# Kernel tuning notes

Hardware: AMD Instinct MI355X
Metric: run time of the kernel (lower is better)

## Reference

```python
import jax, jax.numpy as jnp
import numpy as np

HEADS = 48
HEAD_DIM = 64
DIM = 3072
RANK = 128
TEXT_LEN = 226
VID_LEN = 1822
B = 1
LORA_W = 1.0
EPS = 1e-5


def setup_inputs() -> dict:
    key = jax.random.key(0)
    ks = jax.random.split(key, 24)
    s = 0.02  # weight init scale
    inp = {
        "hidden_states": jax.random.normal(ks[0], (B, VID_LEN, DIM), jnp.float32),
        "encoder_hidden_states": jax.random.normal(ks[1], (B, TEXT_LEN, DIM), jnp.float32),
        "rope_cos": jax.random.uniform(ks[2], (VID_LEN, HEAD_DIM), jnp.float32),
        "rope_sin": jax.random.uniform(ks[3], (VID_LEN, HEAD_DIM), jnp.float32),
        "Wq": jax.random.normal(ks[4], (DIM, DIM), jnp.float32) * s,
        "bq": jax.random.normal(ks[5], (DIM,), jnp.float32) * s,
        "Wk": jax.random.normal(ks[6], (DIM, DIM), jnp.float32) * s,
        "bk": jax.random.normal(ks[7], (DIM,), jnp.float32) * s,
        "Wv": jax.random.normal(ks[8], (DIM, DIM), jnp.float32) * s,
        "bv": jax.random.normal(ks[9], (DIM,), jnp.float32) * s,
        "Wo": jax.random.normal(ks[10], (DIM, DIM), jnp.float32) * s,
        "bo": jax.random.normal(ks[11], (DIM,), jnp.float32) * s,
        "lq_down": jax.random.normal(ks[12], (RANK, DIM), jnp.float32) / RANK,
        "lq_up": jax.random.normal(ks[13], (DIM, RANK), jnp.float32) * s,
        "lk_down": jax.random.normal(ks[14], (RANK, DIM), jnp.float32) / RANK,
        "lk_up": jax.random.normal(ks[15], (DIM, RANK), jnp.float32) * s,
        "lv_down": jax.random.normal(ks[16], (RANK, DIM), jnp.float32) / RANK,
        "lv_up": jax.random.normal(ks[17], (DIM, RANK), jnp.float32) * s,
        "lp_down": jax.random.normal(ks[18], (RANK, DIM), jnp.float32) / RANK,
        "lp_up": jax.random.normal(ks[19], (DIM, RANK), jnp.float32) * s,
        "gamma_q": jnp.ones((HEAD_DIM,), jnp.float32),
        "beta_q": jnp.zeros((HEAD_DIM,), jnp.float32),
        "gamma_k": jnp.ones((HEAD_DIM,), jnp.float32),
        "beta_k": jnp.zeros((HEAD_DIM,), jnp.float32),
    }
    return inp


def _lora(x, down, up):
    # x: [B,S,DIM]; down: [RANK,DIM]; up: [DIM,RANK]
    return (x @ down.T) @ up.T


def _layernorm(x, gamma, beta):
    mu = jnp.mean(x, axis=-1, keepdims=True)
    var = jnp.mean(jnp.square(x - mu), axis=-1, keepdims=True)
    return (x - mu) * jax.lax.rsqrt(var + EPS) * gamma + beta


def _apply_rope(x, cos, sin):
    # diffusers apply_rotary_emb, use_real=True, unbind_dim=-1
    # x: [B,H,S,D]; cos/sin: [S,D]
    xr = x.reshape(*x.shape[:-1], HEAD_DIM // 2, 2)
    x1, x2 = xr[..., 0], xr[..., 1]
    x_rot = jnp.stack([-x2, x1], axis=-1).reshape(x.shape)
    return x * cos + x_rot * sin


def reference(hidden_states, encoder_hidden_states, rope_cos, rope_sin,
              Wq, bq, Wk, bk, Wv, bv, Wo, bo,
              lq_down, lq_up, lk_down, lk_up, lv_down, lv_up, lp_down, lp_up,
              gamma_q, beta_q, gamma_k, beta_k):
    h = jnp.concatenate([encoder_hidden_states, hidden_states], axis=1)  # [B,S,DIM]
    S = h.shape[1]

    q = h @ Wq.T + bq + _lora(h, lq_down, lq_up) * LORA_W
    k = h @ Wk.T + bk + _lora(h, lk_down, lk_up) * LORA_W
    v = h @ Wv.T + bv + _lora(h, lv_down, lv_up) * LORA_W

    def split_heads(x):  # [B,S,DIM] -> [B,H,S,D]
        return x.reshape(B, S, HEADS, HEAD_DIM).transpose(0, 2, 1, 3)

    q, k, v = split_heads(q), split_heads(k), split_heads(v)
    q = _layernorm(q, gamma_q, beta_q)
    k = _layernorm(k, gamma_k, beta_k)

    # RoPE on video tokens only
    q = q.at[:, :, TEXT_LEN:].set(_apply_rope(q[:, :, TEXT_LEN:], rope_cos, rope_sin))
    k = k.at[:, :, TEXT_LEN:].set(_apply_rope(k[:, :, TEXT_LEN:], rope_cos, rope_sin))

    # scaled dot-product attention (no mask, no dropout)
    scale = 1.0 / np.sqrt(HEAD_DIM).astype(np.float32)
    scores = jnp.einsum("bhqd,bhkd->bhqk", q, k) * scale
    probs = jax.nn.softmax(scores, axis=-1)
    attn_out = jnp.einsum("bhqk,bhkd->bhqd", probs, v)

    out = attn_out.transpose(0, 2, 1, 3).reshape(B, S, DIM)
    out = out @ Wo.T + bo + _lora(out, lp_down, lp_up) * LORA_W

    enc_out = out[:, :TEXT_LEN, :]
    hid_out = out[:, TEXT_LEN:, :]
    return (hid_out, enc_out)
```

## Files before the change

### kernel.cpp

```cpp
#include <hip/hip_runtime.h>
#include <hip/hip_bf16.h>
#include <stdint.h>

#define S_TOT 2048
#define TEXT 226
#define VID 1822
#define DIM 3072
#define NH 48
#define HD 64

typedef __bf16 bf16x8 __attribute__((ext_vector_type(8)));
typedef __bf16 bf16x4 __attribute__((ext_vector_type(4)));
typedef float f32x4 __attribute__((ext_vector_type(4)));

#define AS1 __attribute__((address_space(1)))
#define AS3 __attribute__((address_space(3)))

__device__ __forceinline__ void g2l16(const void* g, void* l) {
    __builtin_amdgcn_global_load_lds((const AS1 uint32_t*)(uintptr_t)g,
                                     (AS3 uint32_t*)(uintptr_t)l, 16, 0, 0);
}

__device__ __forceinline__ f32x4 mfma16(bf16x4 a, bf16x4 b, f32x4 c) {
#if __has_builtin(__builtin_amdgcn_mfma_f32_16x16x16bf16_1k)
    typedef short s4 __attribute__((ext_vector_type(4)));
    union U { bf16x4 b; s4 s; };
    U ua, ub; ua.b = a; ub.b = b;
    return __builtin_amdgcn_mfma_f32_16x16x16bf16_1k(ua.s, ub.s, c, 0, 0, 0);
#else
    f32x4 d = c;
    asm volatile("v_mfma_f32_16x16x16_bf16 %0, %1, %2, %0"
                 : "+v"(d) : "v"(a), "v"(b));
    return d;
#endif
}

#define ARENA_N 47431680ull

struct NormArgs { const void* p[24]; };

__global__ __launch_bounds__(256)
void normalize_inputs(NormArgs a, __bf16* __restrict__ arena)
{
    static constexpr unsigned long long segStart[25] = {
        0ull, 694272ull, 6291456ull, 15728640ull, 25165824ull, 34603008ull,
        44040192ull, 44433408ull, 44826624ull, 45219840ull, 45613056ull,
        46006272ull, 46399488ull, 46792704ull, 47185920ull, 47302528ull,
        47419136ull, 47422208ull, 47425280ull, 47428352ull, 47431424ull,
        47431488ull, 47431552ull, 47431616ull, 47431680ull };
    static constexpr int segIn[24] = {
        1, 0, 4, 6, 8, 10, 12, 13, 14, 15, 16, 17, 18, 19, 2, 3,
        5, 7, 9, 11, 20, 21, 22, 23 };

    const uint32_t w0 = *(const uint32_t*)a.p[20];
    const bool f32in = (w0 == 0x3F800000u);

    const size_t i0 = ((size_t)blockIdx.x * 256 + threadIdx.x) * 8;
    if (i0 >= ARENA_N) return;
    int s = 0;
    while (i0 >= segStart[s + 1]) s++;
    const size_t off = i0 - segStart[s];

    if (f32in) {
        const float* src = (const float*)a.p[segIn[s]] + off;
        const float4 v0 = ((const float4*)src)[0];
        const float4 v1 = ((const float4*)src)[1];
        bf16x8 o;
        o[0] = (__bf16)v0.x; o[1] = (__bf16)v0.y; o[2] = (__bf16)v0.z; o[3] = (__bf16)v0.w;
        o[4] = (__bf16)v1.x; o[5] = (__bf16)v1.y; o[6] = (__bf16)v1.z; o[7] = (__bf16)v1.w;
        *(bf16x8*)(arena + i0) = o;
    } else {
        const __bf16* src = (const __bf16*)a.p[segIn[s]] + off;
        *(uint4*)(arena + i0) = *(const uint4*)src;
    }
}

__device__ __forceinline__ void mm_chunks(
    const __bf16* __restrict__ Ag, int lda, const __bf16* __restrict__ Bg, int ldb,
    int kbeg, int kend, f32x4 (&acc)[4][4], __bf16* As, __bf16* Bs,
    int wave, int srow, int schk, int rdoff, int l15, int wm, int wn)
{
    for (int k0 = kbeg; k0 < kend; k0 += 32) {
        __syncthreads();
#pragma unroll
        for (int i = 0; i < 2; i++) {
            const int blk = i * 4 + wave;
            const int r = blk * 16 + srow;
            g2l16(Ag + (size_t)r * lda + k0 + schk, &As[blk * 512]);
            g2l16(Bg + (size_t)r * ldb + k0 + schk, &Bs[blk * 512]);
        }
        __syncthreads();
        bf16x8 af[4], bfr[4];
#pragma unroll
        for (int i = 0; i < 4; i++)
            af[i] = *(const bf16x8*)&As[(wm + i * 16 + l15) * 32 + rdoff];
#pragma unroll
        for (int j = 0; j < 4; j++)
            bfr[j] = *(const bf16x8*)&Bs[(wn + j * 16 + l15) * 32 + rdoff];
#pragma unroll
        for (int i = 0; i < 4; i++)
#pragma unroll
            for (int j = 0; j < 4; j++)
                acc[i][j] = __builtin_amdgcn_mfma_f32_16x16x32_bf16(af[i], bfr[j], acc[i][j], 0, 0, 0);
    }
}

template<int MODE>
__global__ __launch_bounds__(256)
void gemm_bt(const __bf16* __restrict__ A, int lda,
             const __bf16* __restrict__ B0, const __bf16* __restrict__ B1,
             const __bf16* __restrict__ B2, int ldb,
             const __bf16* __restrict__ bias0, const __bf16* __restrict__ bias1,
             const __bf16* __restrict__ bias2,
             __bf16* __restrict__ Cb, int ldc, int K, int tilesPerGroup,
             void* __restrict__ dout, const void* __restrict__ probe)
{
    __shared__ __bf16 As[128 * 32];
    __shared__ __bf16 Bs[128 * 32];
    const int tid  = threadIdx.x;
    const int wave = tid >> 6;
    const int lane = tid & 63;
    const int l15  = lane & 15, quad = lane >> 4;
    const int bm = blockIdx.x, bn = blockIdx.y;
    const int group = bn / tilesPerGroup;
    const int nt    = bn - group * tilesPerGroup;
    const __bf16* B    = (group == 0) ? B0 : ((group == 1) ? B1 : B2);
    const __bf16* bias = (group == 0) ? bias0 : ((group == 1) ? bias1 : bias2);

    const int srow  = lane >> 2;
    const int schk  = ((((lane & 3) - (lane >> 3)) & 3)) * 8;
    const int rdoff = ((quad + (l15 >> 1)) & 3) * 8;
    const __bf16* Ag = A + (size_t)(bm * 128) * lda;
    const __bf16* Bg = B + (size_t)(nt * 128) * ldb;

    f32x4 acc[4][4] = {};
    const int wm = (wave & 1) * 64;
    const int wn = (wave >> 1) * 64;

    mm_chunks(Ag, lda, Bg, ldb, 0, K, acc, As, Bs, wave, srow, schk, rdoff, l15, wm, wn);

    bool f32out = false;
    if (MODE == 1) f32out = (*(const uint32_t*)probe == 0x3F800000u);

#pragma unroll
    for (int i = 0; i < 4; i++) {
#pragma unroll
        for (int j = 0; j < 4; j++) {
            const int coll = wn + j * 16 + l15;
            const int col  = bn * 128 + coll;
            float bv = 0.f;
            if (bias) bv = (float)bias[nt * 128 + coll];
#pragma unroll
            for (int r = 0; r < 4; r++) {
                const int row = bm * 128 + wm + i * 16 + quad * 4 + r;
                float v = acc[i][j][r] + bv;
                if (MODE == 1) {
                    const size_t mrow = (row < TEXT) ? (size_t)(row + VID) : (size_t)(row - TEXT);
                    if (f32out) ((float*)dout)[mrow * DIM + col] = v;
                    else        ((__bf16*)dout)[mrow * DIM + col] = (__bf16)v;
                } else {
                    Cb[(size_t)row * ldc + col] = (__bf16)v;
                }
            }
        }
    }
}

#define QKV_NT 48
#define QKV_NI 24

__device__ __forceinline__ void barx() {
    asm volatile("" ::: "memory");
    __builtin_amdgcn_s_barrier();
    asm volatile("" ::: "memory");
}
__device__ __forceinline__ void vmw6() { asm volatile("s_waitcnt vmcnt(6)" ::: "memory"); }
__device__ __forceinline__ void vmw0() { asm volatile("s_waitcnt vmcnt(0)" ::: "memory"); }

__device__ __forceinline__ void stage2(const __bf16* gsrc, __bf16* lds, size_t koff) {
    g2l16(gsrc + koff,      lds);
    g2l16(gsrc + koff + 32, lds + 8192);
}

__global__ __launch_bounds__(512)
void gemm256_qkv(const __bf16* __restrict__ A,
                 const __bf16* __restrict__ B0, const __bf16* __restrict__ B1,
                 const __bf16* __restrict__ B2,
                 const __bf16* __restrict__ bias0, const __bf16* __restrict__ bias1,
                 const __bf16* __restrict__ bias2,
                 __bf16* __restrict__ C)
{
    __shared__ __bf16 L[65536];

    const int bid = blockIdx.x;
    const int swz = (bid & 7) * 32 + (bid >> 3);
    const int bm = swz & 7;
    const int bn = swz >> 3;
    const int group = bn / 12;
    const int nt    = bn - group * 12;
    const __bf16* Bm   = (group == 0) ? B0 : ((group == 1) ? B1 : B2);
    const __bf16* bias = (group == 0) ? bias0 : ((group == 1) ? bias1 : bias2);

    const int tid = threadIdx.x, wave = tid >> 6, lane = tid & 63;
    const int wr = wave >> 2, wc = wave & 3;
    const int l15 = lane & 15, quad = lane >> 4;
    const int srow  = lane >> 2;
    const int schk  = ((((lane & 3) - (lane >> 3)) & 3)) * 8;
    const int rdoff = ((quad + (l15 >> 1)) & 3) * 8;
    const int rdbase = l15 * 32 + rdoff;

    static constexpr int AL0[8] = {0,1,2,3, 8,9,10,11};
    static constexpr int AL1[8] = {4,5,6,7, 12,13,14,15};
    static constexpr int BL0[8] = {0,1,4,5, 8,9,12,13};
    static constexpr int BL1[8] = {2,3,6,7, 10,11,14,15};
    const int a0 = AL0[wave], a1 = AL1[wave], b0 = BL0[wave], b1 = BL1[wave];

    const __bf16* Ag = A  + (size_t)(bm * 256) * DIM;
    const __bf16* Bg = Bm + (size_t)(nt * 256) * DIM;
    const __bf16* gA0 = Ag + (size_t)(a0 * 16 + srow) * DIM + schk;
    const __bf16* gA1 = Ag + (size_t)(a1 * 16 + srow) * DIM + schk;
    const __bf16* gB0 = Bg + (size_t)(b0 * 16 + srow) * DIM + schk;
    const __bf16* gB1 = Bg + (size_t)(b1 * 16 + srow) * DIM + schk;

#define STG_A0(BUF, T) stage2(gA0, &L[(BUF)*32768 +         a0*512], (size_t)(T)*64)
#define STG_A1(BUF, T) stage2(gA1, &L[(BUF)*32768 +         a1*512], (size_t)(T)*64)
#define STG_B0(BUF, T) stage2(gB0, &L[(BUF)*32768 + 16384 + b0*512], (size_t)(T)*64)
#define STG_B1(BUF, T) stage2(gB1, &L[(BUF)*32768 + 16384 + b1*512], (size_t)(T)*64)

    f32x4 acc[8][4] = {};

    STG_A0(0, 0); STG_B0(0, 0); STG_A1(0, 0); STG_B1(0, 0);
    STG_A0(1, 1); STG_B0(1, 1); STG_A1(1, 1);
    vmw6();
    barx();

#define PH(BUF, MH, NH, STAGE, WAIT) do {                                        \
    bf16x8 af[4][2], bfr[2][2];                                                  \
    _Pragma("unroll")                                                            \
    for (int mm = 0; mm < 4; mm++) {                                             \
        af[mm][0] = *(const bf16x8*)&L[(BUF)*32768 +        (wr*8 + (MH)*4 + mm)*512 + rdbase]; \
        af[mm][1] = *(const bf16x8*)&L[(BUF)*32768 + 8192 + (wr*8 + (MH)*4 + mm)*512 + rdbase]; \
    }                                                                            \
    _Pragma("unroll")                                                            \
    for (int nn = 0; nn < 2; nn++) {                                             \
        bfr[nn][0] = *(const bf16x8*)&L[(BUF)*32768 + 16384 +        (wc*4 + (NH)*2 + nn)*512 + rdbase]; \
        bfr[nn][1] = *(const bf16x8*)&L[(BUF)*32768 + 16384 + 8192 + (wc*4 + (NH)*2 + nn)*512 + rdbase]; \
    }                                                                            \
    barx();                                                                      \
    STAGE;                                                                       \
    __builtin_amdgcn_s_setprio(1);                                               \
    _Pragma("unroll")                                                            \
    for (int mm = 0; mm < 4; mm++)                                               \
        _Pragma("unroll")                                                        \
        for (int nn = 0; nn < 2; nn++) {                                         \
            acc[(MH)*4+mm][(NH)*2+nn] = __builtin_amdgcn_mfma_f32_16x16x32_bf16( \
                af[mm][0], bfr[nn][0], acc[(MH)*4+mm][(NH)*2+nn], 0, 0, 0);      \
            acc[(MH)*4+mm][(NH)*2+nn] = __builtin_amdgcn_mfma_f32_16x16x32_bf16( \
                af[mm][1], bfr[nn][1], acc[(MH)*4+mm][(NH)*2+nn], 0, 0, 0);      \
        }                                                                        \
    __builtin_amdgcn_s_setprio(0);                                               \
    WAIT;                                                                        \
    barx();                                                                      \
} while (0)

#pragma unroll 1
    for (int i = 0; i < QKV_NI; i++) {
        const int t1 = 2 * i + 1, t2 = 2 * i + 2, t3 = 2 * i + 3;
        const bool more = (i < QKV_NI - 1);
        PH(0, 0, 0, { STG_B1(1, t1); },              { });
        PH(0, 0, 1, { if (more) STG_A0(0, t2); },    { });
        PH(0, 1, 0, { if (more) STG_B0(0, t2); },    { });
        PH(0, 1, 1, { if (more) STG_A1(0, t2); },    { if (more) vmw6(); else vmw0(); });
        PH(1, 0, 0, { if (more) STG_B1(0, t2); },    { });
        PH(1, 0, 1, { if (more) STG_A0(1, t3); },    { });
        PH(1, 1, 0, { if (more) STG_B0(1, t3); },    { });
        PH(1, 1, 1, { if (more) STG_A1(1, t3); },    { if (more) vmw6(); else vmw0(); });
    }
#undef PH
#undef STG_A0
#undef STG_A1
#undef STG_B0
#undef STG_B1

#pragma unroll
    for (int mh = 0; mh < 2; mh++)
#pragma unroll
    for (int nh = 0; nh < 2; nh++)
#pragma unroll
    for (int nn = 0; nn < 2; nn++) {
        const int coll = wc * 64 + nh * 32 + nn * 16 + l15;
        const float bv = (float)bias[nt * 256 + coll];
        const int col = bn * 256 + coll;
#pragma unroll
        for (int mm = 0; mm < 4; mm++) {
            const int rowb = bm * 256 + wr * 128 + mh * 64 + mm * 16 + quad * 4;
#pragma unroll
            for (int r = 0; r < 4; r++)
                C[(size_t)(rowb + r) * 9216 + col] = (__bf16)(acc[mh*4+mm][nh*2+nn][r] + bv);
        }
    }
}

struct TpArgs { const __bf16* S[4]; __bf16* D[4]; };

__global__ __launch_bounds__(256)
void transp_ld(TpArgs a)
{
    __shared__ float tile[64][65];
    const __bf16* src = a.S[blockIdx.z];
    __bf16* dst = a.D[blockIdx.z];
    const int j0 = blockIdx.x * 64;
    const int r0 = blockIdx.y * 64;
    const int tid = threadIdx.x;
    const int rr = tid >> 4;
    const int cc = (tid & 15) * 4;
#pragma unroll
    for (int p = 0; p < 4; p++) {
        const int r = p * 16 + rr;
        const uint2 raw = *(const uint2*)&src[(size_t)(r0 + r) * DIM + j0 + cc];
        const __bf16* b = (const __bf16*)&raw;
#pragma unroll
        for (int e = 0; e < 4; e++) tile[r][cc + e] = (float)b[e];
    }
    __syncthreads();
#pragma unroll
    for (int p = 0; p < 4; p++) {
        const int j = p * 16 + rr;
        __bf16 o[4];
#pragma unroll
        for (int e = 0; e < 4; e++) o[e] = (__bf16)tile[cc + e][j];
        *(uint2*)&dst[(size_t)(j0 + j) * 128 + r0 + cc] = *(const uint2*)o;
    }
}

struct FoldArgs { const __bf16* A[4]; const __bf16* B[4]; const __bf16* W[4]; __bf16* D[4]; };

__global__ __launch_bounds__(256)
void fold_w(FoldArgs a)
{
    __shared__ __bf16 As[128 * 32];
    __shared__ __bf16 Bs[128 * 32];
    const int z = blockIdx.z;
    const int tid  = threadIdx.x;
    const int wave = tid >> 6;
    const int lane = tid & 63;
    const int l15  = lane & 15, quad = lane >> 4;
    const int bm = blockIdx.x, bn = blockIdx.y;

    const int srow  = lane >> 2;
    const int schk  = ((((lane & 3) - (lane >> 3)) & 3)) * 8;
    const int rdoff = ((quad + (l15 >> 1)) & 3) * 8;
    const __bf16* Ag = a.A[z] + (size_t)(bm * 128) * 128;
    const __bf16* Bg = a.B[z] + (size_t)(bn * 128) * 128;
    const __bf16* W  = a.W[z];
    __bf16* D = a.D[z];

    f32x4 acc[4][4] = {};
    const int wm = (wave & 1) * 64;
    const int wn = (wave >> 1) * 64;

    mm_chunks(Ag, 128, Bg, 128, 0, 128, acc, As, Bs, wave, srow, schk, rdoff, l15, wm, wn);

#pragma unroll
    for (int i = 0; i < 4; i++) {
#pragma unroll
        for (int j = 0; j < 4; j++) {
            const int col = bn * 128 + wn + j * 16 + l15;
#pragma unroll
            for (int r = 0; r < 4; r++) {
                const int row = bm * 128 + wm + i * 16 + quad * 4 + r;
                const size_t idx = (size_t)row * DIM + col;
                D[idx] = (__bf16)(acc[i][j][r] + (float)W[idx]);
            }
        }
    }
}

__global__ __launch_bounds__(256)
void ln_vt(const __bf16* __restrict__ qkv,
           const __bf16* __restrict__ gq, const __bf16* __restrict__ bq,
           const __bf16* __restrict__ gk, const __bf16* __restrict__ bk,
           const __bf16* __restrict__ cosb, const __bf16* __restrict__ sinb,
           __bf16* __restrict__ qh, __bf16* __restrict__ kh,
           __bf16* __restrict__ vt)
{
    __shared__ float tile[64][65];
    if (blockIdx.x < 2048) {
        const int s = blockIdx.x;
        const int wave = threadIdx.x >> 6, lane = threadIdx.x & 63;
        for (int idx = wave; idx < 2 * NH; idx += 4) {
            const int mat  = idx / NH;
            const int head = idx - mat * NH;
            float x = (float)qkv[(size_t)s * 9216 + mat * DIM + head * HD + lane];
            float mu = x;
            mu += __shfl_xor(mu, 1, 64);  mu += __shfl_xor(mu, 2, 64);
            mu += __shfl_xor(mu, 4, 64);  mu += __shfl_xor(mu, 8, 64);
            mu += __shfl_xor(mu, 16, 64); mu += __shfl_xor(mu, 32, 64);
            mu *= 0.015625f;
            float d = x - mu;
            float vv = d * d;
            vv += __shfl_xor(vv, 1, 64);  vv += __shfl_xor(vv, 2, 64);
            vv += __shfl_xor(vv, 4, 64);  vv += __shfl_xor(vv, 8, 64);
            vv += __shfl_xor(vv, 16, 64); vv += __shfl_xor(vv, 32, 64);
            vv *= 0.015625f;
            const float g = (float)(mat ? gk[lane] : gq[lane]);
            const float b = (float)(mat ? bk[lane] : bq[lane]);
            float y = d * rsqrtf(vv + 1e-5f) * g + b;
            if (s >= TEXT) {
                const int pos = s - TEXT;
                const float c  = (float)cosb[pos * HD + lane];
                const float sn = (float)sinb[pos * HD + lane];
                const float oth = __shfl_xor(y, 1, 64);
                const float rot = (lane & 1) ? oth : -oth;
                y = y * c + rot * sn;
            }
            if (mat == 0) y *= 0.125f;
            __bf16* dst = mat ? kh : qh;
            dst[((size_t)head * S_TOT + s) * HD + lane] = (__bf16)y;
        }
    } else {
        const int vb = blockIdx.x - 2048;
        const int h = vb >> 5, sb = vb & 31;
        const int tid = threadIdx.x;
        const int r0 = tid >> 4;
        const int c0 = (tid & 15) * 4;
#pragma unroll
        for (int p = 0; p < 4; p++) {
            const int r = p * 16 + r0;
            const uint2 raw = *(const uint2*)&qkv[((size_t)(sb * 64 + r)) * 9216 + 2 * DIM + h * HD + c0];
            const __bf16* b = (const __bf16*)&raw;
#pragma unroll
            for (int e = 0; e < 4; e++) tile[r][c0 + e] = (float)b[e];
        }
        __syncthreads();
#pragma unroll
        for (int p = 0; p < 4; p++) {
            const int d = p * 16 + r0;
            __bf16 o[4];
#pragma unroll
            for (int e = 0; e < 4; e++) o[e] = (__bf16)tile[c0 + e][d];
            *(uint2*)&vt[((size_t)(h * HD + d)) * S_TOT + sb * 64 + c0] = *(const uint2*)o;
        }
    }
}

#define KS_LD 72
#define VS_LD 136
#define NKB (S_TOT / 128)

__device__ __forceinline__ void fa_load(const __bf16* __restrict__ kh,
                                        const __bf16* __restrict__ vt,
                                        int h, int kb, int tid,
                                        bf16x8 (&kr)[4], bf16x8 (&vr)[4])
{
#pragma unroll
    for (int p = 0; p < 4; p++) {
        const int id = p * 256 + tid;
        const int krow = id >> 3, kc = (id & 7) * 8;
        kr[p] = *(const bf16x8*)(kh + ((size_t)(h * S_TOT + kb * 128 + krow)) * HD + kc);
        const int vrow = id >> 4, vc = (id & 15) * 8;
        vr[p] = *(const bf16x8*)(vt + ((size_t)(h * HD + vrow)) * S_TOT + kb * 128 + vc);
    }
}

__global__ __launch_bounds__(256)
void flash_attn(const __bf16* __restrict__ qh, const __bf16* __restrict__ kh,
                const __bf16* __restrict__ vt, __bf16* __restrict__ outp)
{
    __shared__ __bf16 Ks[128 * KS_LD];
    __shared__ __bf16 Vs[64 * VS_LD];
    const int qb = blockIdx.x, h = blockIdx.y;
    const int tid = threadIdx.x, wave = tid >> 6, lane = tid & 63;
    const int l15 = lane & 15, quad = lane >> 4;

    const __bf16* qp = qh + ((size_t)(h * S_TOT + qb * 64 + wave * 16 + l15)) * HD + quad * 8;
    const bf16x8 qf0 = *(const bf16x8*)qp;
    const bf16x8 qf1 = *(const bf16x8*)(qp + 32);

    f32x4 of[4] = {};
    float m_i = -1e30f, l_i = 0.f;
    const float L2E = 1.44269504f;

    bf16x8 kr[4], vr[4];
    fa_load(kh, vt, h, 0, tid, kr, vr);

    for (int kb = 0; kb < NKB; kb++) {
        __syncthreads();
#pragma unroll
        for (int p = 0; p < 4; p++) {
            const int id = p * 256 + tid;
            const int krow = id >> 3, kc = (id & 7) * 8;
            *(bf16x8*)&Ks[krow * KS_LD + kc] = kr[p];
            const int vrow = id >> 4, vc = (id & 15) * 8;
            *(bf16x8*)&Vs[vrow * VS_LD + vc] = vr[p];
        }
        __syncthreads();
        if (kb + 1 < NKB) fa_load(kh, vt, h, kb + 1, tid, kr, vr);

        f32x4 sf[8];
#pragma unroll
        for (int n = 0; n < 8; n++) {
            const bf16x8 k0 = *(const bf16x8*)&Ks[(n * 16 + l15) * KS_LD + quad * 8];
            const bf16x8 k1 = *(const bf16x8*)&Ks[(n * 16 + l15) * KS_LD + 32 + quad * 8];
            f32x4 z = {0.f, 0.f, 0.f, 0.f};
            z = __builtin_amdgcn_mfma_f32_16x16x32_bf16(k0, qf0, z, 0, 0, 0);
            sf[n] = __builtin_amdgcn_mfma_f32_16x16x32_bf16(k1, qf1, z, 0, 0, 0);
        }

        float mx = sf[0][0];
#pragma unroll
        for (int n = 0; n < 8; n++)
#pragma unroll
            for (int r = 0; r < 4; r++) mx = fmaxf(mx, sf[n][r]);
        mx = fmaxf(mx, __shfl_xor(mx, 16, 64));
        mx = fmaxf(mx, __shfl_xor(mx, 32, 64));
        const float mnew = fmaxf(m_i, mx);
        const float alpha = __builtin_amdgcn_exp2f((m_i - mnew) * L2E);
        m_i = mnew;
        float rs = 0.f;
#pragma unroll
        for (int n = 0; n < 8; n++)
#pragma unroll
            for (int r = 0; r < 4; r++) {
                const float pv = __builtin_amdgcn_exp2f((sf[n][r] - mnew) * L2E);
                sf[n][r] = pv;
                rs += pv;
            }
        rs += __shfl_xor(rs, 16, 64);
        rs += __shfl_xor(rs, 32, 64);
        l_i = l_i * alpha + rs;

        bf16x4 pf[8];
#pragma unroll
        for (int kk = 0; kk < 8; kk++) {
            bf16x4 o;
            o[0] = (__bf16)sf[kk][0]; o[1] = (__bf16)sf[kk][1];
            o[2] = (__bf16)sf[kk][2]; o[3] = (__bf16)sf[kk][3];
            pf[kk] = o;
        }

#pragma unroll
        for (int r = 0; r < 4; r++) {
            const float a_r = __shfl(alpha, quad * 4 + r, 16);
#pragma unroll
            for (int j = 0; j < 4; j++) of[j][r] *= a_r;
        }

#pragma unroll
        for (int kk = 0; kk < 8; kk++) {
#pragma unroll
            for (int j = 0; j < 4; j++) {
                const bf16x4 vf = *(const bf16x4*)&Vs[(j * 16 + l15) * VS_LD + kk * 16 + quad * 4];
                of[j] = mfma16(pf[kk], vf, of[j]);
            }
        }
    }

#pragma unroll
    for (int r = 0; r < 4; r++) {
        const float lr = __shfl(l_i, quad * 4 + r, 16);
        const float inv = 1.f / lr;
        const int row = qb * 64 + wave * 16 + quad * 4 + r;
#pragma unroll
        for (int j = 0; j < 4; j++)
            outp[(size_t)row * DIM + h * HD + j * 16 + l15] = (__bf16)(of[j][r] * inv);
    }
}

extern "C" void kernel_launch(void* const* d_in, const int* in_sizes, int n_in,
                              void* d_out, int out_size, void* d_ws, size_t ws_size,
                              hipStream_t stream)
{
    char* ws = (char*)d_ws;
    __bf16* arena = (__bf16*)ws;

    const __bf16* h     = arena + 0;
    const __bf16* Wq    = arena + 6291456;
    const __bf16* Wk    = arena + 15728640;
    const __bf16* Wv    = arena + 25165824;
    const __bf16* Wo    = arena + 34603008;
    const __bf16* lqd   = arena + 44040192;
    const __bf16* lqu   = arena + 44433408;
    const __bf16* lkd   = arena + 44826624;
    const __bf16* lku   = arena + 45219840;
    const __bf16* lvd   = arena + 45613056;
    const __bf16* lvu   = arena + 46006272;
    const __bf16* lpd   = arena + 46399488;
    const __bf16* lpu   = arena + 46792704;
    const __bf16* ropec = arena + 47185920;
    const __bf16* ropes = arena + 47302528;
    const __bf16* bq    = arena + 47419136;
    const __bf16* bk    = arena + 47422208;
    const __bf16* bv    = arena + 47425280;
    const __bf16* bo    = arena + 47428352;
    const __bf16* gq    = arena + 47431424;
    const __bf16* btq   = arena + 47431488;
    const __bf16* gk    = arena + 47431552;
    const __bf16* btk   = arena + 47431616;

    __bf16* ldT  = (__bf16*)(ws + 94863360);
    __bf16* qkvb = (__bf16*)(ws + 98009088);
    __bf16* Wpo  = (__bf16*)(ws + 135757824);
    __bf16* Wpq  = (__bf16*)(ws + 154632192);
    __bf16* Wpk  = (__bf16*)(ws + 173506560);
    __bf16* Wpv  = (__bf16*)(ws + 192380928);
    __bf16* qh   = (__bf16*)(ws + 154632192);
    __bf16* kh   = (__bf16*)(ws + 179798016);
    __bf16* vt   = (__bf16*)(ws + 12582912);
    __bf16* attn = (__bf16*)(ws + 0);

    NormArgs na;
    for (int i = 0; i < 24; i++) na.p[i] = d_in[i];
    normalize_inputs<<<(unsigned)((ARENA_N / 8 + 255) / 256), 256, 0, stream>>>(na, arena);

    TpArgs tp;
    tp.S[0] = lqd; tp.S[1] = lkd; tp.S[2] = lvd; tp.S[3] = lpd;
    tp.D[0] = ldT; tp.D[1] = ldT + 393216; tp.D[2] = ldT + 786432; tp.D[3] = ldT + 1179648;
    transp_ld<<<dim3(48, 2, 4), 256, 0, stream>>>(tp);

    FoldArgs fa;
    fa.A[0] = lqu; fa.A[1] = lku; fa.A[2] = lvu; fa.A[3] = lpu;
    fa.B[0] = tp.D[0]; fa.B[1] = tp.D[1]; fa.B[2] = tp.D[2]; fa.B[3] = tp.D[3];
    fa.W[0] = Wq; fa.W[1] = Wk; fa.W[2] = Wv; fa.W[3] = Wo;
    fa.D[0] = Wpq; fa.D[1] = Wpk; fa.D[2] = Wpv; fa.D[3] = Wpo;
    fold_w<<<dim3(24, 24, 4), 256, 0, stream>>>(fa);

    gemm256_qkv<<<256, 512, 0, stream>>>(h, Wpq, Wpk, Wpv, bq, bk, bv, qkvb);
    gemm_bt<3><<<dim3(16, 8), 256, 0, stream>>>(
        h, DIM, Wpv + (size_t)2048 * DIM, Wpv + (size_t)2048 * DIM, Wpv + (size_t)2048 * DIM,
        DIM, bv + 2048, bv + 2048, bv + 2048,
        qkvb + 8192, 9216, DIM, 8, nullptr, nullptr);

    ln_vt<<<2048 + 1536, 256, 0, stream>>>(qkvb, gq, btq, gk, btk, ropec, ropes, qh, kh, vt);

    flash_attn<<<dim3(32, 48), 256, 0, stream>>>(qh, kh, vt, attn);

    gemm_bt<1><<<dim3(16, 24), 256, 0, stream>>>(
        attn, DIM, Wpo, Wpo, Wpo, DIM, bo, bo, bo,
        nullptr, DIM, DIM, 24, d_out, d_in[20]);
}
```

Before: 712.7 us.

## Process two query tiles per flash-attention block and fold log2e into Q scale

Each flash-attention block now handles 128 query rows as two 64-row passes that share each staged K/V tile, halving the grid and the K/V global-to-LDS traffic per query. The softmax scale now includes log2(e) in the Q prescale, which removes the per-element multiply before exp2. Launch bounds request 3 blocks per CU. The cost is more registers for two sets of accumulators and fewer blocks (768) to spread across CUs.

```diff
diff --git a/kernel.cpp b/kernel.cpp
--- a/kernel.cpp
+++ b/kernel.cpp
@@ -414,7 +414,7 @@
                 const float rot = (lane & 1) ? oth : -oth;
                 y = y * c + rot * sn;
             }
-            if (mat == 0) y *= 0.125f;
+            if (mat == 0) y *= 0.1803368801111137f;
             __bf16* dst = mat ? kh : qh;
             dst[((size_t)head * S_TOT + s) * HD + lane] = (__bf16)y;
         }
@@ -463,23 +463,89 @@
     }
 }
 
-__global__ __launch_bounds__(256)
+__device__ __forceinline__ void fa_pass(const __bf16* __restrict__ Ks,
+                                        const __bf16* __restrict__ Vs,
+                                        bf16x8 qf0, bf16x8 qf1,
+                                        f32x4 (&of)[4], float& m_i, float& l_i,
+                                        int l15, int quad)
+{
+    f32x4 sf[8];
+#pragma unroll
+    for (int n = 0; n < 8; n++) {
+        const bf16x8 k0 = *(const bf16x8*)&Ks[(n * 16 + l15) * KS_LD + quad * 8];
+        const bf16x8 k1 = *(const bf16x8*)&Ks[(n * 16 + l15) * KS_LD + 32 + quad * 8];
+        f32x4 z = {0.f, 0.f, 0.f, 0.f};
+        z = __builtin_amdgcn_mfma_f32_16x16x32_bf16(k0, qf0, z, 0, 0, 0);
+        sf[n] = __builtin_amdgcn_mfma_f32_16x16x32_bf16(k1, qf1, z, 0, 0, 0);
+    }
+
+    float mx = fmaxf(fmaxf(sf[0][0], sf[0][1]), fmaxf(sf[0][2], sf[0][3]));
+#pragma unroll
+    for (int n = 1; n < 8; n++)
+        mx = fmaxf(mx, fmaxf(fmaxf(sf[n][0], sf[n][1]), fmaxf(sf[n][2], sf[n][3])));
+    mx = fmaxf(mx, __shfl_xor(mx, 16, 64));
+    mx = fmaxf(mx, __shfl_xor(mx, 32, 64));
+    const float mnew = fmaxf(m_i, mx);
+    const float alpha = __builtin_amdgcn_exp2f(m_i - mnew);
+    m_i = mnew;
+    float rs = 0.f;
+#pragma unroll
+    for (int n = 0; n < 8; n++)
+#pragma unroll
+        for (int r = 0; r < 4; r++) {
+            const float pv = __builtin_amdgcn_exp2f(sf[n][r] - mnew);
+            sf[n][r] = pv;
+            rs += pv;
+        }
+    rs += __shfl_xor(rs, 16, 64);
+    rs += __shfl_xor(rs, 32, 64);
+    l_i = l_i * alpha + rs;
+
+    bf16x4 pf[8];
+#pragma unroll
+    for (int kk = 0; kk < 8; kk++) {
+        bf16x4 o;
+        o[0] = (__bf16)sf[kk][0]; o[1] = (__bf16)sf[kk][1];
+        o[2] = (__bf16)sf[kk][2]; o[3] = (__bf16)sf[kk][3];
+        pf[kk] = o;
+    }
+
+#pragma unroll
+    for (int r = 0; r < 4; r++) {
+        const float a_r = __shfl(alpha, quad * 4 + r, 16);
+#pragma unroll
+        for (int j = 0; j < 4; j++) of[j][r] *= a_r;
+    }
+
+#pragma unroll
+    for (int kk = 0; kk < 8; kk++) {
+#pragma unroll
+        for (int j = 0; j < 4; j++) {
+            const bf16x4 vf = *(const bf16x4*)&Vs[(j * 16 + l15) * VS_LD + kk * 16 + quad * 4];
+            of[j] = mfma16(pf[kk], vf, of[j]);
+        }
+    }
+}
+
+__global__ __launch_bounds__(256, 3)
 void flash_attn(const __bf16* __restrict__ qh, const __bf16* __restrict__ kh,
                 const __bf16* __restrict__ vt, __bf16* __restrict__ outp)
 {
     __shared__ __bf16 Ks[128 * KS_LD];
     __shared__ __bf16 Vs[64 * VS_LD];
-    const int qb = blockIdx.x, h = blockIdx.y;
+    const int qb2 = blockIdx.x, h = blockIdx.y;
     const int tid = threadIdx.x, wave = tid >> 6, lane = tid & 63;
     const int l15 = lane & 15, quad = lane >> 4;
 
-    const __bf16* qp = qh + ((size_t)(h * S_TOT + qb * 64 + wave * 16 + l15)) * HD + quad * 8;
-    const bf16x8 qf0 = *(const bf16x8*)qp;
-    const bf16x8 qf1 = *(const bf16x8*)(qp + 32);
-
-    f32x4 of[4] = {};
-    float m_i = -1e30f, l_i = 0.f;
-    const float L2E = 1.44269504f;
+    const __bf16* qp = qh + ((size_t)(h * S_TOT + qb2 * 128 + wave * 16 + l15)) * HD + quad * 8;
+    const bf16x8 qf0a = *(const bf16x8*)qp;
+    const bf16x8 qf1a = *(const bf16x8*)(qp + 32);
+    const bf16x8 qf0b = *(const bf16x8*)(qp + 64 * HD);
+    const bf16x8 qf1b = *(const bf16x8*)(qp + 64 * HD + 32);
+
+    f32x4 ofa[4] = {}, ofb[4] = {};
+    float m_a = -1e30f, l_a = 0.f;
+    float m_b = -1e30f, l_b = 0.f;
 
     bf16x8 kr[4], vr[4];
     fa_load(kh, vt, h, 0, tid, kr, vr);
@@ -495,75 +561,26 @@
             *(bf16x8*)&Vs[vrow * VS_LD + vc] = vr[p];
         }
         __syncthreads();
+
+        fa_pass(Ks, Vs, qf0a, qf1a, ofa, m_a, l_a, l15, quad);
         if (kb + 1 < NKB) fa_load(kh, vt, h, kb + 1, tid, kr, vr);
-
-        f32x4 sf[8];
-#pragma unroll
-        for (int n = 0; n < 8; n++) {
-            const bf16x8 k0 = *(const bf16x8*)&Ks[(n * 16 + l15) * KS_LD + quad * 8];
-            const bf16x8 k1 = *(const bf16x8*)&Ks[(n * 16 + l15) * KS_LD + 32 + quad * 8];
-            f32x4 z = {0.f, 0.f, 0.f, 0.f};
-            z = __builtin_amdgcn_mfma_f32_16x16x32_bf16(k0, qf0, z, 0, 0, 0);
-            sf[n] = __builtin_amdgcn_mfma_f32_16x16x32_bf16(k1, qf1, z, 0, 0, 0);
-        }
-
-        float mx = sf[0][0];
-#pragma unroll
-        for (int n = 0; n < 8; n++)
-#pragma unroll
-            for (int r = 0; r < 4; r++) mx = fmaxf(mx, sf[n][r]);
-        mx = fmaxf(mx, __shfl_xor(mx, 16, 64));
-        mx = fmaxf(mx, __shfl_xor(mx, 32, 64));
-        const float mnew = fmaxf(m_i, mx);
-        const float alpha = __builtin_amdgcn_exp2f((m_i - mnew) * L2E);
-        m_i = mnew;
-        float rs = 0.f;
-#pragma unroll
-        for (int n = 0; n < 8; n++)
-#pragma unroll
-            for (int r = 0; r < 4; r++) {
-                const float pv = __builtin_amdgcn_exp2f((sf[n][r] - mnew) * L2E);
-                sf[n][r] = pv;
-                rs += pv;
-            }
-        rs += __shfl_xor(rs, 16, 64);
-        rs += __shfl_xor(rs, 32, 64);
-        l_i = l_i * alpha + rs;
-
-        bf16x4 pf[8];
-#pragma unroll
-        for (int kk = 0; kk < 8; kk++) {
-            bf16x4 o;
-            o[0] = (__bf16)sf[kk][0]; o[1] = (__bf16)sf[kk][1];
-            o[2] = (__bf16)sf[kk][2]; o[3] = (__bf16)sf[kk][3];
-            pf[kk] = o;
-        }
-
-#pragma unroll
-        for (int r = 0; r < 4; r++) {
-            const float a_r = __shfl(alpha, quad * 4 + r, 16);
-#pragma unroll
-            for (int j = 0; j < 4; j++) of[j][r] *= a_r;
-        }
-
-#pragma unroll
-        for (int kk = 0; kk < 8; kk++) {
-#pragma unroll
-            for (int j = 0; j < 4; j++) {
-                const bf16x4 vf = *(const bf16x4*)&Vs[(j * 16 + l15) * VS_LD + kk * 16 + quad * 4];
-                of[j] = mfma16(pf[kk], vf, of[j]);
-            }
-        }
+        fa_pass(Ks, Vs, qf0b, qf1b, ofb, m_b, l_b, l15, quad);
     }
 
 #pragma unroll
     for (int r = 0; r < 4; r++) {
-        const float lr = __shfl(l_i, quad * 4 + r, 16);
-        const float inv = 1.f / lr;
-        const int row = qb * 64 + wave * 16 + quad * 4 + r;
+        const float lra = __shfl(l_a, quad * 4 + r, 16);
+        const float inva = 1.f / lra;
+        const int rowa = qb2 * 128 + wave * 16 + quad * 4 + r;
 #pragma unroll
         for (int j = 0; j < 4; j++)
-            outp[(size_t)row * DIM + h * HD + j * 16 + l15] = (__bf16)(of[j][r] * inv);
+            outp[(size_t)rowa * DIM + h * HD + j * 16 + l15] = (__bf16)(ofa[j][r] * inva);
+        const float lrb = __shfl(l_b, quad * 4 + r, 16);
+        const float invb = 1.f / lrb;
+        const int rowb = rowa + 64;
+#pragma unroll
+        for (int j = 0; j < 4; j++)
+            outp[(size_t)rowb * DIM + h * HD + j * 16 + l15] = (__bf16)(ofb[j][r] * invb);
     }
 }
 
@@ -633,7 +650,7 @@
 
     ln_vt<<<2048 + 1536, 256, 0, stream>>>(qkvb, gq, btq, gk, btk, ropec, ropes, qh, kh, vt);
 
-    flash_attn<<<dim3(32, 48), 256, 0, stream>>>(qh, kh, vt, attn);
+    flash_attn<<<dim3(16, 48), 256, 0, stream>>>(qh, kh, vt, attn);
 
     gemm_bt<1><<<dim3(16, 24), 256, 0, stream>>>(
         attn, DIM, Wpo, Wpo, Wpo, DIM, bo, bo, bo,
```

After: 1.026 ms. +43.9%, slower.
